# Optimization experiments

Measured on AMD Instinct MI355X. Metric: run time of the kernel, lower is better.

The kernel has to match this reference:

```python
import jax, jax.numpy as jnp
import numpy as np

N_ATOMS = 100_000
N_PAIRS = 6_400_000
N_BATCH = 16


def smooth_switch(x, x0, x1):
    t = (x - x0) / (x1 - x0)
    tc = jnp.clip(t, 1e-9, 1.0 - 1e-9)  # safe interior values
    f1 = jnp.exp(-1.0 / tc)
    f2 = jnp.exp(-1.0 / (1.0 - tc))
    s = f1 / (f1 + f2)
    return jnp.where(t <= 0.0, 0.0, jnp.where(t >= 1.0, 1.0, s))


def setup_inputs() -> dict:
    key = jax.random.key(0)
    k1, k2, k3, k4, k5 = jax.random.split(key, 5)
    atomic_numbers = jax.random.randint(k1, (N_ATOMS,), 1, 81).astype(jnp.float32)
    # displacements scaled so distances span the (0, 10) switch window
    displacements = jax.random.normal(k2, (N_PAIRS, 3), dtype=jnp.float32) * 2.5
    idx_i = jnp.sort(jax.random.randint(k3, (N_PAIRS,), 0, N_ATOMS)).astype(jnp.int32)
    idx_j = jax.random.randint(k4, (N_PAIRS,), 0, N_ATOMS).astype(jnp.int32)
    atom_mask = jnp.ones((N_ATOMS,), dtype=jnp.float32)
    batch_mask = jnp.ones((N_PAIRS,), dtype=jnp.float32)
    batch_segments = jnp.sort(jax.random.randint(k5, (N_ATOMS,), 0, N_BATCH)).astype(jnp.int32)
    # ZBL parameters (non-trainable constants in the module)
    a_coefficient = jnp.asarray(0.8854, dtype=jnp.float32)
    a_exponent = jnp.asarray(0.23, dtype=jnp.float32)
    phi_coefficients = jnp.asarray([0.18175, 0.50986, 0.28022, 0.02817], dtype=jnp.float32)
    phi_exponents = jnp.asarray([3.1998, 0.94229, 0.4029, 0.20162], dtype=jnp.float32)
    return {
        "atomic_numbers": atomic_numbers,
        "displacements": displacements,
        "idx_i": idx_i,
        "idx_j": idx_j,
        "atom_mask": atom_mask,
        "batch_mask": batch_mask,
        "batch_segments": batch_segments,
        "batch_size": N_BATCH,
        "a_coefficient": a_coefficient,
        "a_exponent": a_exponent,
        "phi_coefficients": phi_coefficients,
        "phi_exponents": phi_exponents,
    }


def reference(atomic_numbers, displacements, idx_i, idx_j, atom_mask, batch_mask,
              batch_segments, batch_size, a_coefficient, a_exponent,
              phi_coefficients, phi_exponents):
    n_atoms = atomic_numbers.shape[0]
    displacements = displacements + (1.0 - batch_mask[..., None])
    distances = jnp.maximum(jnp.linalg.norm(displacements, axis=-1), 1e-10)  # [P]
    switch_off = smooth_switch(distances, 0.0, 10.0)

    safe_atomic_numbers = jnp.maximum(atomic_numbers, 1e-06)
    za = jnp.exp(jnp.log(safe_atomic_numbers) * jnp.abs(a_exponent))
    za = jnp.nan_to_num(za, nan=1e-06, posinf=1e6, neginf=1e-06)
    za_sum = za[idx_i] + za[idx_j]                     # [P]
    denominator = jnp.maximum(za_sum, 1e-06)
    a_ij = jnp.abs(a_coefficient) / denominator
    a_ij = jnp.nan_to_num(a_ij, nan=1e-06, posinf=1e6, neginf=1e-06)
    arguments = jnp.maximum(distances, 1e-10) / jnp.maximum(a_ij, 1e-10)
    arguments = jnp.nan_to_num(arguments, nan=1e-06, posinf=1e6, neginf=1e-06)

    raw_coefficients = jnp.abs(phi_coefficients)
    coefficients = raw_coefficients / jnp.maximum(jnp.sum(raw_coefficients), 1e-10)
    exponents = jnp.maximum(jnp.abs(phi_exponents), 1e-10)
    log_terms = -exponents[None, :] * arguments[:, None]          # [P,4]
    max_log = jnp.max(log_terms, axis=1, keepdims=True)           # [P,1]
    exp_terms = jnp.exp(log_terms - max_log)
    exp_terms = jnp.nan_to_num(exp_terms, nan=0.0, posinf=1.0, neginf=0.0)
    phi = jnp.sum(coefficients[None, :] * exp_terms, axis=1) * jnp.exp(max_log)[..., 0]
    phi = jnp.maximum(phi, 1e-30)
    phi = jnp.nan_to_num(phi, nan=1e-30, posinf=1e6, neginf=1e-30)

    safe_distances = jnp.maximum(distances, 1e-10)
    safe_phi = jnp.maximum(phi, 1e-30)
    safe_switch = jnp.maximum(switch_off, 1e-30)
    charge_product = jnp.minimum(safe_atomic_numbers[idx_i] * safe_atomic_numbers[idx_j], 1e4)
    base_repulsion = jnp.minimum(0.5 * charge_product / safe_distances, 1e6)
    repulsion = base_repulsion * safe_phi * safe_switch
    repulsion = jnp.clip(repulsion, 0.0, 1e6)
    repulsion = jnp.nan_to_num(repulsion, nan=0.0, posinf=1e6, neginf=0.0)
    repulsion = repulsion * batch_mask

    Erep = jax.ops.segment_sum(repulsion, segment_ids=idx_i, num_segments=n_atoms)
    Erep = Erep * atom_mask
    Erep = jnp.clip(Erep, 0.0, 1e6)
    Erep = jnp.nan_to_num(Erep, nan=0.0, posinf=1e6, neginf=0.0)
    Erep = Erep * 0.01
    return Erep[..., None, None, None]  # [N,1,1,1]
```

## Files before the change

kernel.cpp:

```cpp
#include <hip/hip_runtime.h>
#include <math.h>


#define LOG2E 1.4426950408889634f
#define BLK   1024
#define NBLK  256
#define STRD  (2 * BLK)
#define CAP   2048

static __device__ __forceinline__ float rcpf_(float x)  { return __builtin_amdgcn_rcpf(x); }
static __device__ __forceinline__ float rsqf_(float x)  { return __builtin_amdgcn_rsqf(x); }
static __device__ __forceinline__ float exp2f_(float x) { return __builtin_amdgcn_exp2f(x); }
static __device__ __forceinline__ float log2f_(float x) { return __builtin_amdgcn_logf(x); }

struct f3 { float x, y, z; };
struct G  { int ii, jj; float bm, dx, dy, dz; };

__global__ void zbl_k0(const float* __restrict__ an,
                       unsigned char* __restrict__ z8,
                       float* __restrict__ out, int n) {
    int i = blockIdx.x * blockDim.x + threadIdx.x;
    if (i >= n) return;
    int z = (int)(an[i] + 0.5f);
    z8[i] = (unsigned char)min(max(z, 1), 255);
    out[i] = 0.0f;
}

static __device__ __forceinline__ G loadG(const int* __restrict__ idx_i,
                                          const int* __restrict__ idx_j,
                                          const float* __restrict__ bmk,
                                          const float* __restrict__ disp,
                                          int p, int cend) {
    G g; g.ii = -1; g.jj = 0; g.bm = 0.0f; g.dx = 0.0f; g.dy = 0.0f; g.dz = 0.0f;
    if (p < cend) {
        g.ii = idx_i[p];
        g.jj = idx_j[p];
        g.bm = bmk[p];
        f3 d = *reinterpret_cast<const f3*>(disp + (long)p * 3);
        g.dx = d.x; g.dy = d.y; g.dz = d.z;
    }
    return g;
}

__global__ __launch_bounds__(BLK) void zbl_pair_kernel(
    const float* __restrict__ disp,
    const int*   __restrict__ idx_i,
    const int*   __restrict__ idx_j,
    const float* __restrict__ batch_mask,
    const unsigned char* __restrict__ z8g,
    const float* __restrict__ a_coef_ptr,
    const float* __restrict__ a_exp_ptr,
    const float* __restrict__ phi_c,
    const float* __restrict__ phi_e,
    float* __restrict__ out_acc,
    int nA, int nP)
{
    extern __shared__ unsigned char smem[];
    const int nA_pad = (nA + 15) & ~15;
    unsigned char* s_z8  = smem;
    float*         s_za  = (float*)(smem + nA_pad);
    float*         s_acc = (float*)(smem + nA_pad + 1024);

    const int tid = threadIdx.x;

    {
        const int nw = nA >> 4;
        const uint4* g4 = reinterpret_cast<const uint4*>(z8g);
        uint4* s4 = reinterpret_cast<uint4*>(s_z8);
        for (int i = tid; i < nw; i += BLK) s4[i] = g4[i];
        for (int i = (nw << 4) + tid; i < nA; i += BLK) s_z8[i] = z8g[i];
    }
    if (tid < 256) {
        float ae = fabsf(a_exp_ptr[0]);
        int z = max(tid, 1);
        s_za[tid] = exp2f_(ae * log2f_((float)z));
    }
    for (int i = tid; i < CAP; i += BLK) s_acc[i] = 0.0f;

    const float ac_inv = rcpf_(fmaxf(fabsf(a_coef_ptr[0]), 1e-10f));
    float c0 = fabsf(phi_c[0]), c1 = fabsf(phi_c[1]);
    float c2 = fabsf(phi_c[2]), c3 = fabsf(phi_c[3]);
    const float cinv = rcpf_(fmaxf(c0 + c1 + c2 + c3, 1e-10f));
    c0 *= cinv; c1 *= cinv; c2 *= cinv; c3 *= cinv;
    const float e0 = fmaxf(fabsf(phi_e[0]), 1e-10f);
    const float e1 = fmaxf(fabsf(phi_e[1]), 1e-10f);
    const float e2 = fmaxf(fabsf(phi_e[2]), 1e-10f);
    const float e3 = fmaxf(fabsf(phi_e[3]), 1e-10f);

    int chunk = (nP + NBLK - 1) / NBLK;
    chunk = (chunk + STRD - 1) & ~(STRD - 1);
    const int cbeg = blockIdx.x * chunk;
    const int cend = min(cbeg + chunk, nP);
    const int lane = tid & 63;
    const int kbase = (cbeg < nP) ? idx_i[cbeg] : 0;

    __syncthreads();

#define COMPUTE_G(g, rep, key)                                                  \
    {                                                                           \
        rep = 0.0f; key = -1;                                                   \
        if ((g).ii >= 0) {                                                      \
            const int zi = (int)s_z8[(g).ii];                                   \
            const int zj = (int)s_z8[(g).jj];                                   \
            const float za_i = s_za[zi];                                        \
            const float za_j = s_za[zj];                                        \
            const float add = 1.0f - (g).bm;                                    \
            const float dx = (g).dx + add, dy = (g).dy + add, dz = (g).dz + add;\
            float d2   = fmaxf(dx * dx + dy * dy + dz * dz, 1e-20f);            \
            float rsq  = rsqf_(d2);                                             \
            float dist = d2 * rsq;                                              \
            float tt = dist * 0.1f;                                             \
            float tc = fminf(fmaxf(tt, 1e-9f), 1.0f - 1e-9f);                   \
            float u  = (1.0f - 2.0f * tc) * rcpf_(tc - tc * tc);                \
            float s  = rcpf_(1.0f + exp2f_(u * LOG2E));                         \
            float sw = (tt >= 1.0f) ? 1.0f : s;                                 \
            float za_sum = za_i + za_j;                                         \
            float arg  = fminf(dist * za_sum * ac_inv, 1e6f);                   \
            float narg = -arg * LOG2E;                                          \
            float phi  = c0 * exp2f_(e0 * narg) + c1 * exp2f_(e1 * narg) +      \
                         c2 * exp2f_(e2 * narg) + c3 * exp2f_(e3 * narg);       \
            phi = fminf(fmaxf(phi, 1e-30f), 1e6f);                              \
            float cp   = fminf((float)(zi * zj), 1e4f);                         \
            float brep = fminf(0.5f * cp * rsq, 1e6f);                          \
            float r    = brep * phi * fmaxf(sw, 1e-30f);                        \
            r = fminf(fmaxf(r, 0.0f), 1e6f);                                    \
            if (!(r == r)) r = 0.0f;                                            \
            rep = r * (g).bm;                                                   \
            key = (g).ii;                                                       \
        }                                                                       \
    }

#define DEPOSIT(k, v)                                                           \
    {                                                                           \
        int slot = (k) - kbase;                                                 \
        if (slot < CAP) atomicAdd(&s_acc[slot], (v));                           \
        else            atomicAdd(&out_acc[k], (v));                            \
    }

#define REDUCE_G(rep, key)                                                      \
    {                                                                           \
        const int k0_ = __shfl(key, 0);                                         \
        if (__all(key == k0_)) {                                                \
            float v = rep;                                                      \
            _Pragma("unroll")                                                   \
            for (int d = 1; d < 64; d <<= 1) v += __shfl_xor(v, d);             \
            if (lane == 0 && k0_ >= 0) DEPOSIT(k0_, v);                         \
        } else {                                                                \
            float v = rep;                                                      \
            int   k = key;                                                      \
            _Pragma("unroll")                                                   \
            for (int d = 1; d < 64; d <<= 1) {                                  \
                float nv = __shfl_down(v, d);                                   \
                int   nk = __shfl_down(k, d);                                   \
                if (lane + d < 64 && nk == k) v += nv;                          \
            }                                                                   \
            int pk = __shfl_up(k, 1);                                           \
            bool head = (lane == 0) || (pk != k);                               \
            if (head && k >= 0) DEPOSIT(k, v);                                  \
        }                                                                       \
    }

    G a0 = loadG(idx_i, idx_j, batch_mask, disp, cbeg + tid,              cend);
    G b0 = loadG(idx_i, idx_j, batch_mask, disp, cbeg + BLK + tid,        cend);
    G a1 = loadG(idx_i, idx_j, batch_mask, disp, cbeg + STRD + tid,       cend);
    G b1 = loadG(idx_i, idx_j, batch_mask, disp, cbeg + STRD + BLK + tid, cend);

    for (int pb = cbeg; pb < cend; pb += STRD) {
        G a2 = loadG(idx_i, idx_j, batch_mask, disp, pb + 2 * STRD + tid,       cend);
        G b2 = loadG(idx_i, idx_j, batch_mask, disp, pb + 2 * STRD + BLK + tid, cend);

        float repA, repB; int keyA, keyB;
        COMPUTE_G(a0, repA, keyA);
        COMPUTE_G(b0, repB, keyB);
        REDUCE_G(repA, keyA);
        REDUCE_G(repB, keyB);

        a0 = a1; b0 = b1; a1 = a2; b1 = b2;
    }
#undef COMPUTE_G
#undef REDUCE_G
#undef DEPOSIT

    __syncthreads();
    for (int s = tid; s < CAP; s += BLK) {
        float v = s_acc[s];
        int   k = kbase + s;
        if (v != 0.0f && k < nA) atomicAdd(&out_acc[k], v);
    }
}

__global__ void zbl_epilogue(float* __restrict__ out,
                             const float* __restrict__ atom_mask, int n) {
    int i = blockIdx.x * blockDim.x + threadIdx.x;
    if (i >= n) return;
    float v = out[i] * atom_mask[i];
    v = fminf(fmaxf(v, 0.0f), 1e6f);
    if (!(v == v)) v = 0.0f;
    out[i] = v * 0.01f;
}

extern "C" void kernel_launch(void* const* d_in, const int* in_sizes, int n_in,
                              void* d_out, int out_size, void* d_ws, size_t ws_size,
                              hipStream_t stream) {
    const float* an         = (const float*)d_in[0];
    const float* disp       = (const float*)d_in[1];
    const int*   idx_i      = (const int*)d_in[2];
    const int*   idx_j      = (const int*)d_in[3];
    const float* atom_mask  = (const float*)d_in[4];
    const float* batch_mask = (const float*)d_in[5];
    const float* a_coef     = (const float*)d_in[8];
    const float* a_exp      = (const float*)d_in[9];
    const float* phi_c      = (const float*)d_in[10];
    const float* phi_e      = (const float*)d_in[11];

    const int nA = in_sizes[0];
    const int nP = in_sizes[2];
    float* out = (float*)d_out;

    unsigned char* z8 = (unsigned char*)d_ws;

    zbl_k0<<<(nA + 255) / 256, 256, 0, stream>>>(an, z8, out, nA);

    const int nA_pad = (nA + 15) & ~15;
    const size_t smem = (size_t)nA_pad + 1024 + (size_t)CAP * sizeof(float);
    zbl_pair_kernel<<<NBLK, BLK, smem, stream>>>(
        disp, idx_i, idx_j, batch_mask, z8, a_coef, a_exp, phi_c, phi_e,
        out, nA, nP);

    zbl_epilogue<<<(nA + 255) / 256, 256, 0, stream>>>(out, atom_mask, nA);
}
```

Baseline: 44.58 us.

## Partition pairs by atom range and fuse epilogue into pair kernel

Each block now owns a contiguous range of atoms and locates its pair range by binary search on the sorted idx_i, so every partial sum lands in shared memory. This removes the global atomics, the separate output zeroing, and the epilogue kernel, because each block writes its final masked and scaled outputs directly. Blocks now do uneven amounts of work, since pairs per atom vary, and each block runs a global binary search at startup.

```diff
diff --git a/kernel.cpp b/kernel.cpp
--- a/kernel.cpp
+++ b/kernel.cpp
@@ -6,7 +6,7 @@
 #define BLK   1024
 #define NBLK  256
 #define STRD  (2 * BLK)
-#define CAP   2048
+#define CAP   1024
 
 static __device__ __forceinline__ float rcpf_(float x)  { return __builtin_amdgcn_rcpf(x); }
 static __device__ __forceinline__ float rsqf_(float x)  { return __builtin_amdgcn_rsqf(x); }
@@ -17,13 +17,11 @@
 struct G  { int ii, jj; float bm, dx, dy, dz; };
 
 __global__ void zbl_k0(const float* __restrict__ an,
-                       unsigned char* __restrict__ z8,
-                       float* __restrict__ out, int n) {
+                       unsigned char* __restrict__ z8, int n) {
     int i = blockIdx.x * blockDim.x + threadIdx.x;
     if (i >= n) return;
     int z = (int)(an[i] + 0.5f);
     z8[i] = (unsigned char)min(max(z, 1), 255);
-    out[i] = 0.0f;
 }
 
 static __device__ __forceinline__ G loadG(const int* __restrict__ idx_i,
@@ -42,18 +40,29 @@
     return g;
 }
 
+static __device__ __forceinline__ int lower_bound_i(const int* __restrict__ arr,
+                                                    int n, int val) {
+    int lo = 0, hi = n;
+    while (lo < hi) {
+        int mid = (lo + hi) >> 1;
+        if (arr[mid] < val) lo = mid + 1; else hi = mid;
+    }
+    return lo;
+}
+
 __global__ __launch_bounds__(BLK) void zbl_pair_kernel(
     const float* __restrict__ disp,
     const int*   __restrict__ idx_i,
     const int*   __restrict__ idx_j,
     const float* __restrict__ batch_mask,
     const unsigned char* __restrict__ z8g,
+    const float* __restrict__ atom_mask,
     const float* __restrict__ a_coef_ptr,
     const float* __restrict__ a_exp_ptr,
     const float* __restrict__ phi_c,
     const float* __restrict__ phi_e,
-    float* __restrict__ out_acc,
-    int nA, int nP)
+    float* __restrict__ out,
+    int nA, int nP, int aPerBlk)
 {
     extern __shared__ unsigned char smem[];
     const int nA_pad = (nA + 15) & ~15;
@@ -87,12 +96,11 @@
     const float e2 = fmaxf(fabsf(phi_e[2]), 1e-10f);
     const float e3 = fmaxf(fabsf(phi_e[3]), 1e-10f);
 
-    int chunk = (nP + NBLK - 1) / NBLK;
-    chunk = (chunk + STRD - 1) & ~(STRD - 1);
-    const int cbeg = blockIdx.x * chunk;
-    const int cend = min(cbeg + chunk, nP);
+    const int aBeg = min((int)blockIdx.x * aPerBlk, nA);
+    const int aEnd = min(aBeg + aPerBlk, nA);
+    const int cbeg = lower_bound_i(idx_i, nP, aBeg);
+    const int cend = lower_bound_i(idx_i, nP, aEnd);
     const int lane = tid & 63;
-    const int kbase = (cbeg < nP) ? idx_i[cbeg] : 0;
 
     __syncthreads();
 
@@ -130,13 +138,6 @@
         }                                                                       \
     }
 
-#define DEPOSIT(k, v)                                                           \
-    {                                                                           \
-        int slot = (k) - kbase;                                                 \
-        if (slot < CAP) atomicAdd(&s_acc[slot], (v));                           \
-        else            atomicAdd(&out_acc[k], (v));                            \
-    }
-
 #define REDUCE_G(rep, key)                                                      \
     {                                                                           \
         const int k0_ = __shfl(key, 0);                                         \
@@ -144,7 +145,7 @@
             float v = rep;                                                      \
             _Pragma("unroll")                                                   \
             for (int d = 1; d < 64; d <<= 1) v += __shfl_xor(v, d);             \
-            if (lane == 0 && k0_ >= 0) DEPOSIT(k0_, v);                         \
+            if (lane == 0 && k0_ >= 0) atomicAdd(&s_acc[k0_ - aBeg], v);        \
         } else {                                                                \
             float v = rep;                                                      \
             int   k = key;                                                      \
@@ -156,7 +157,7 @@
             }                                                                   \
             int pk = __shfl_up(k, 1);                                           \
             bool head = (lane == 0) || (pk != k);                               \
-            if (head && k >= 0) DEPOSIT(k, v);                                  \
+            if (head && k >= 0) atomicAdd(&s_acc[k - aBeg], v);                 \
         }                                                                       \
     }
 
@@ -179,24 +180,15 @@
     }
 #undef COMPUTE_G
 #undef REDUCE_G
-#undef DEPOSIT
 
     __syncthreads();
-    for (int s = tid; s < CAP; s += BLK) {
-        float v = s_acc[s];
-        int   k = kbase + s;
-        if (v != 0.0f && k < nA) atomicAdd(&out_acc[k], v);
-    }
-}
-
-__global__ void zbl_epilogue(float* __restrict__ out,
-                             const float* __restrict__ atom_mask, int n) {
-    int i = blockIdx.x * blockDim.x + threadIdx.x;
-    if (i >= n) return;
-    float v = out[i] * atom_mask[i];
-    v = fminf(fmaxf(v, 0.0f), 1e6f);
-    if (!(v == v)) v = 0.0f;
-    out[i] = v * 0.01f;
+    for (int s = tid; s < aEnd - aBeg; s += BLK) {
+        const int a = aBeg + s;
+        float v = s_acc[s] * atom_mask[a];
+        v = fminf(fmaxf(v, 0.0f), 1e6f);
+        if (!(v == v)) v = 0.0f;
+        out[a] = v * 0.01f;
+    }
 }
 
 extern "C" void kernel_launch(void* const* d_in, const int* in_sizes, int n_in,
@@ -219,13 +211,17 @@
 
     unsigned char* z8 = (unsigned char*)d_ws;
 
-    zbl_k0<<<(nA + 255) / 256, 256, 0, stream>>>(an, z8, out, nA);
-
+    zbl_k0<<<(nA + 255) / 256, 256, 0, stream>>>(an, z8, nA);
+
+    int nblk = NBLK;
+    int aPerBlk = (nA + nblk - 1) / nblk;
+    if (aPerBlk > CAP) {
+        nblk = (nA + CAP - 1) / CAP;
+        aPerBlk = CAP;
+    }
     const int nA_pad = (nA + 15) & ~15;
     const size_t smem = (size_t)nA_pad + 1024 + (size_t)CAP * sizeof(float);
-    zbl_pair_kernel<<<NBLK, BLK, smem, stream>>>(
-        disp, idx_i, idx_j, batch_mask, z8, a_coef, a_exp, phi_c, phi_e,
-        out, nA, nP);
-
-    zbl_epilogue<<<(nA + 255) / 256, 256, 0, stream>>>(out, atom_mask, nA);
-}
+    zbl_pair_kernel<<<nblk, BLK, smem, stream>>>(
+        disp, idx_i, idx_j, batch_mask, z8, atom_mask,
+        a_coef, a_exp, phi_c, phi_e, out, nA, nP, aPerBlk);
+}
```

After: 48.77 us. 9.4% more time.
